# Optimization experiments

Measured on AMD Instinct MI355X. Metric: run time of the kernel, lower is better.

## Reference

```python
import jax, jax.numpy as jnp
import numpy as np

N = 500000      # total nodes
B = 10000       # number of graphs
D = 256         # node_size == global_size
SLOPE = 0.01    # LeakyReLU negative slope (torch default)

def leaky_relu(x):
    return jnp.where(x >= 0, x, SLOPE * x)

def setup_inputs() -> dict:
    key = jax.random.key(0)
    ks = jax.random.split(key, 10)
    xg_old = jax.random.normal(ks[0], (B, D), dtype=jnp.float32)
    x = jax.random.normal(ks[1], (N, D), dtype=jnp.float32)
    batch = jnp.sort(jax.random.randint(ks[2], (N,), 0, B)).astype(jnp.int64)
    s = 1.0 / np.sqrt(D)
    W_gate = jax.random.uniform(ks[3], (D, 1), minval=-s, maxval=s, dtype=jnp.float32)
    b_gate = jax.random.uniform(ks[4], (1,), minval=-s, maxval=s, dtype=jnp.float32)
    W_feat = jax.random.uniform(ks[5], (D, D), minval=-s, maxval=s, dtype=jnp.float32)
    b_feat = jax.random.uniform(ks[6], (D,), minval=-s, maxval=s, dtype=jnp.float32)
    s2 = 1.0 / np.sqrt(2 * D)
    W_t = jax.random.uniform(ks[7], (2 * D, D), minval=-s2, maxval=s2, dtype=jnp.float32)
    b_t = jax.random.uniform(ks[8], (D,), minval=-s2, maxval=s2, dtype=jnp.float32)
    return {"xg_old": xg_old, "x": x, "batch": batch,
            "W_gate": W_gate, "b_gate": b_gate,
            "W_feat": W_feat, "b_feat": b_feat,
            "W_t": W_t, "b_t": b_t}

def reference(xg_old, x, batch, W_gate, b_gate, W_feat, b_feat, W_t, b_t):
    batch = batch.astype(jnp.int32)
    # AttentionalAggregation: per-graph softmax over gate scores, weighted sum of feats
    gate = x @ W_gate + b_gate                               # [N, 1]
    feat = leaky_relu(x @ W_feat + b_feat)                   # [N, D]
    m = jax.ops.segment_max(gate, batch, num_segments=B)     # [B, 1]
    g = jnp.exp(gate - m[batch])                             # stable exp
    s = jax.ops.segment_sum(g, batch, num_segments=B)        # [B, 1]
    alpha = g / s[batch]                                     # [N, 1]
    xg = jax.ops.segment_sum(alpha * feat, batch, num_segments=B)  # [B, D]
    # concat with old global state, transform, residual
    cat = jnp.concatenate([xg, xg_old], axis=1)              # [B, 2D]
    out = leaky_relu(cat @ W_t + b_t) + xg_old               # [B, D]
    return out
```

## Files before the change

### kernel.cpp

```cpp
#include <hip/hip_runtime.h>
#include <hip/hip_bf16.h>
#include <math.h>

#define D 256
#define FT_STRIDE 72

typedef short v8s __attribute__((ext_vector_type(8)));
typedef float f32x4 __attribute__((ext_vector_type(4)));
typedef float f32x16 __attribute__((ext_vector_type(16)));

__device__ __forceinline__ unsigned short f2b(float f) {
    return __bfloat16_as_ushort(__float2bfloat16(f));
}
__device__ __forceinline__ float b2f(unsigned short u) {
    return __bfloat162float(__ushort_as_bfloat16(u));
}

__global__ void prep_kernel(const int* __restrict__ batch, int* __restrict__ seg_start,
                            const float* __restrict__ Wf, unsigned short* __restrict__ Wb32,
                            const float* __restrict__ Wt, unsigned short* __restrict__ Wtb,
                            float* __restrict__ xg, int N, int B) {
    const int blk = blockIdx.x, tid = threadIdx.x;
    if (blk < 40) {
        int b = blk * 256 + tid;
        if (b > B) return;
        int lo = 0, hi = N;
        while (lo < hi) {
            int mid = (lo + hi) >> 1;
            if (batch[mid] < b) lo = mid + 1; else hi = mid;
        }
        seg_start[b] = lo;
    } else if (blk < 296) {
        int idx = (blk - 40) * 256 + tid;
        int k = idx >> 8, n = idx & 255;
        int lane = ((k >> 3) & 1) * 32 + (n & 31);
        int j = k & 7, kst = k >> 4, ntile = n >> 5;
        Wb32[(((ntile * 16 + kst) * 64) + lane) * 8 + j] = f2b(Wf[k * 256 + n]);
    } else if (blk < 808) {
        int idx = (blk - 296) * 256 + tid;
        int k = idx >> 8, n = idx & 255;
        int ntile = n >> 4, kst = k >> 5;
        int lane = ((k >> 3) & 3) * 16 + (n & 15);
        int j = k & 7;
        Wtb[(((ntile * 16 + kst) * 64) + lane) * 8 + j] = f2b(Wt[k * 256 + n]);
    } else {
        int idx = (blk - 808) * 256 + tid;
        if (idx < 640000) ((float4*)xg)[idx] = make_float4(0.f, 0.f, 0.f, 0.f);
    }
}

template<bool CONV>
__global__ __launch_bounds__(256) void gate_conv_kernel(
    const float* __restrict__ x, const float* __restrict__ Wg,
    const float* __restrict__ bg, float* __restrict__ gate,
    unsigned short* __restrict__ xb16, int N) {
    const int lane = threadIdx.x & 63;
    const int wid = blockIdx.x * 4 + (threadIdx.x >> 6);
    const int nw = gridDim.x * 4;
    const float4 wv = *(const float4*)(Wg + lane * 4);
    const float bgv = bg[0];
    for (int n = wid * 2; n < N; n += nw * 2) {
        const float4 xv0 = *(const float4*)(x + (size_t)n * D + lane * 4);
        const float4 xv1 = *(const float4*)(x + (size_t)(n + 1) * D + lane * 4);
        if (CONV) {
            ushort4 h0 = { f2b(xv0.x), f2b(xv0.y), f2b(xv0.z), f2b(xv0.w) };
            ushort4 h1 = { f2b(xv1.x), f2b(xv1.y), f2b(xv1.z), f2b(xv1.w) };
            *(ushort4*)(xb16 + (size_t)n * D + lane * 4) = h0;
            *(ushort4*)(xb16 + (size_t)(n + 1) * D + lane * 4) = h1;
        }
        float d0 = xv0.x * wv.x + xv0.y * wv.y + xv0.z * wv.z + xv0.w * wv.w;
        float d1 = xv1.x * wv.x + xv1.y * wv.y + xv1.z * wv.z + xv1.w * wv.w;
        #pragma unroll
        for (int off = 32; off; off >>= 1) {
            d0 += __shfl_xor(d0, off, 64);
            d1 += __shfl_xor(d1, off, 64);
        }
        if (lane == 0) { gate[n] = d0 + bgv; gate[n + 1] = d1 + bgv; }
    }
}

__global__ __launch_bounds__(256) void stats_kernel(const float* __restrict__ gate,
                                                    const int* __restrict__ seg_start,
                                                    float* __restrict__ mvec,
                                                    float* __restrict__ invs, int B) {
    int wid = blockIdx.x * 4 + (threadIdx.x >> 6);
    int lane = threadIdx.x & 63;
    if (wid >= B) return;
    int s0 = seg_start[wid], s1 = seg_start[wid + 1];
    float m = -INFINITY;
    for (int i = s0 + lane; i < s1; i += 64) m = fmaxf(m, gate[i]);
    #pragma unroll
    for (int off = 32; off > 0; off >>= 1) m = fmaxf(m, __shfl_xor(m, off, 64));
    float s = 0.f;
    for (int i = s0 + lane; i < s1; i += 64) s += __expf(gate[i] - m);
    #pragma unroll
    for (int off = 32; off > 0; off >>= 1) s += __shfl_xor(s, off, 64);
    if (lane == 0) { mvec[wid] = m; invs[wid] = (s > 0.f) ? 1.f / s : 0.f; }
}

template<bool BF16IN>
__global__ __launch_bounds__(256, 4) void feat_attn_kernel(
    const float* __restrict__ x, const unsigned short* __restrict__ xb16,
    const unsigned short* __restrict__ Wb32,
    const float* __restrict__ bfeat, const float* __restrict__ gate,
    const int* __restrict__ batch, const float* __restrict__ mvec,
    const float* __restrict__ invs, float* __restrict__ xg, int N) {

    __shared__ unsigned short feat_s[256 * FT_STRIDE] __attribute__((aligned(16)));
    __shared__ float alpha_s[64];
    __shared__ int batch_s[64];

    const int tid = threadIdx.x;
    const int n0 = blockIdx.x * 64;

    if (tid < 64) {
        int n = n0 + tid;
        if (n < N) {
            int b = batch[n];
            batch_s[tid] = b;
            alpha_s[tid] = __expf(gate[n] - mvec[b]) * invs[b];
        } else {
            batch_s[tid] = batch[N - 1];
            alpha_s[tid] = 0.f;
        }
    }

    const int w = tid >> 6, lane = tid & 63;
    const int l31 = lane & 31, lh = lane >> 5;

    f32x16 acc[2][2];
    #pragma unroll
    for (int i = 0; i < 2; i++)
        #pragma unroll
        for (int j = 0; j < 2; j++)
            #pragma unroll
            for (int e = 0; e < 16; e++) acc[i][j][e] = 0.f;

    size_t abase[2];
    #pragma unroll
    for (int rt = 0; rt < 2; rt++) {
        int r = n0 + rt * 32 + l31;
        if (r > N - 1) r = N - 1;
        abase[rt] = (size_t)r * D + lh * 8;
    }

    v8s A[3][2], Bf[2][2];
    #pragma unroll
    for (int p = 0; p < 2; p++) {
        #pragma unroll
        for (int rt = 0; rt < 2; rt++) {
            if (BF16IN) A[p][rt] = *(const v8s*)(xb16 + abase[rt] + p * 16);
            else {
                const float* src = x + abase[rt] + p * 16;
                float4 f0 = *(const float4*)src, f1 = *(const float4*)(src + 4);
                v8s v; v[0]=(short)f2b(f0.x); v[1]=(short)f2b(f0.y);
                v[2]=(short)f2b(f0.z); v[3]=(short)f2b(f0.w);
                v[4]=(short)f2b(f1.x); v[5]=(short)f2b(f1.y);
                v[6]=(short)f2b(f1.z); v[7]=(short)f2b(f1.w);
                A[p][rt] = v;
            }
        }
        #pragma unroll
        for (int ct = 0; ct < 2; ct++)
            Bf[p][ct] = *(const v8s*)(Wb32 + (((size_t)(w * 2 + ct) * 16 + p) * 64 + lane) * 8);
    }

    #pragma unroll
    for (int ks = 0; ks < 16; ks++) {
        const int cs = ks % 3, bs = ks & 1;
        if (ks < 14) {
            const int ns = (ks + 2) % 3;
            #pragma unroll
            for (int rt = 0; rt < 2; rt++) {
                if (BF16IN) A[ns][rt] = *(const v8s*)(xb16 + abase[rt] + (ks + 2) * 16);
                else {
                    const float* src = x + abase[rt] + (ks + 2) * 16;
                    float4 f0 = *(const float4*)src, f1 = *(const float4*)(src + 4);
                    v8s v; v[0]=(short)f2b(f0.x); v[1]=(short)f2b(f0.y);
                    v[2]=(short)f2b(f0.z); v[3]=(short)f2b(f0.w);
                    v[4]=(short)f2b(f1.x); v[5]=(short)f2b(f1.y);
                    v[6]=(short)f2b(f1.z); v[7]=(short)f2b(f1.w);
                    A[ns][rt] = v;
                }
            }
        }
        if (ks < 15) {
            const int nb = (ks + 1) & 1;
            #pragma unroll
            for (int ct = 0; ct < 2; ct++)
                Bf[nb][ct] = *(const v8s*)(Wb32 + (((size_t)(w * 2 + ct) * 16 + ks + 1) * 64 + lane) * 8);
        }
        #pragma unroll
        for (int rt = 0; rt < 2; rt++)
            #pragma unroll
            for (int ct = 0; ct < 2; ct++)
                acc[rt][ct] = __builtin_amdgcn_mfma_f32_32x32x16_bf16(
                    A[cs][rt], Bf[bs][ct], acc[rt][ct], 0, 0, 0);
    }

    __syncthreads();

    #pragma unroll
    for (int ct = 0; ct < 2; ct++) {
        int col = w * 64 + ct * 32 + l31;
        float bias = bfeat[col];
        #pragma unroll
        for (int rt = 0; rt < 2; rt++) {
            #pragma unroll
            for (int g = 0; g < 4; g++) {
                int rbase = rt * 32 + g * 8 + 4 * lh;
                ushort4 h;
                #pragma unroll
                for (int rr = 0; rr < 4; rr++) {
                    float y = acc[rt][ct][g * 4 + rr] + bias;
                    y = (y >= 0.f) ? y : 0.01f * y;
                    y *= alpha_s[rbase + rr];
                    ((unsigned short*)&h)[rr] = f2b(y);
                }
                *(ushort4*)(&feat_s[col * FT_STRIDE + rbase]) = h;
            }
        }
    }
    __syncthreads();

    float sum = 0.f;
    int cur = batch_s[0];
    #pragma unroll
    for (int i0 = 0; i0 < 64; i0 += 8) {
        v8s f = *(const v8s*)(&feat_s[tid * FT_STRIDE + i0]);
        int b0 = batch_s[i0], b7 = batch_s[i0 + 7];
        if (b0 == b7) {
            if (b0 != cur) {
                atomicAdd(&xg[(size_t)cur * D + tid], sum);
                sum = 0.f; cur = b0;
            }
            float p0 = b2f((unsigned short)f[0]) + b2f((unsigned short)f[1]);
            float p1 = b2f((unsigned short)f[2]) + b2f((unsigned short)f[3]);
            float p2 = b2f((unsigned short)f[4]) + b2f((unsigned short)f[5]);
            float p3 = b2f((unsigned short)f[6]) + b2f((unsigned short)f[7]);
            sum += (p0 + p1) + (p2 + p3);
        } else {
            #pragma unroll
            for (int j = 0; j < 8; j++) {
                int b = batch_s[i0 + j];
                if (b != cur) {
                    atomicAdd(&xg[(size_t)cur * D + tid], sum);
                    sum = 0.f; cur = b;
                }
                sum += b2f((unsigned short)f[j]);
            }
        }
    }
    atomicAdd(&xg[(size_t)cur * D + tid], sum);
}

__global__ __launch_bounds__(256) void out_mfma_kernel(
    const float* __restrict__ xg, const float* __restrict__ xg_old,
    const unsigned short* __restrict__ Wtb, const float* __restrict__ bt,
    float* __restrict__ out, int B) {
    const int tid = threadIdx.x;
    const int w = tid >> 6, lane = tid & 63, mrow = lane & 15, q = lane >> 4;
    const int r0 = blockIdx.x * 64;

    f32x4 acc[4][4];
    #pragma unroll
    for (int i = 0; i < 4; i++)
        #pragma unroll
        for (int j = 0; j < 4; j++) acc[i][j] = (f32x4){0.f, 0.f, 0.f, 0.f};

    size_t rowbase[4];
    #pragma unroll
    for (int rb = 0; rb < 4; rb++) {
        int r = r0 + rb * 16 + mrow;
        if (r > B - 1) r = B - 1;
        rowbase[rb] = (size_t)r * D + q * 8;
    }

    #pragma unroll
    for (int ks = 0; ks < 16; ks++) {
        v8s a[4], bfr[4];
        #pragma unroll
        for (int rb = 0; rb < 4; rb++) {
            const float* src = (ks < 8) ? (xg + rowbase[rb] + ks * 32)
                                        : (xg_old + rowbase[rb] + (ks - 8) * 32);
            float4 f0 = *(const float4*)src;
            float4 f1 = *(const float4*)(src + 4);
            v8s v;
            v[0] = (short)f2b(f0.x); v[1] = (short)f2b(f0.y);
            v[2] = (short)f2b(f0.z); v[3] = (short)f2b(f0.w);
            v[4] = (short)f2b(f1.x); v[5] = (short)f2b(f1.y);
            v[6] = (short)f2b(f1.z); v[7] = (short)f2b(f1.w);
            a[rb] = v;
        }
        #pragma unroll
        for (int cb = 0; cb < 4; cb++)
            bfr[cb] = *(const v8s*)(Wtb + (((size_t)(w * 4 + cb) * 16 + ks) * 64 + lane) * 8);
        #pragma unroll
        for (int rb = 0; rb < 4; rb++)
            #pragma unroll
            for (int cb = 0; cb < 4; cb++)
                acc[rb][cb] = __builtin_amdgcn_mfma_f32_16x16x32_bf16(
                    a[rb], bfr[cb], acc[rb][cb], 0, 0, 0);
    }

    #pragma unroll
    for (int cb = 0; cb < 4; cb++) {
        int col = w * 64 + cb * 16 + mrow;
        float bias = bt[col];
        #pragma unroll
        for (int rb = 0; rb < 4; rb++) {
            #pragma unroll
            for (int reg = 0; reg < 4; reg++) {
                int row = r0 + rb * 16 + q * 4 + reg;
                if (row < B) {
                    float y = acc[rb][cb][reg] + bias;
                    y = (y >= 0.f) ? y : 0.01f * y;
                    out[(size_t)row * D + col] = y + xg_old[(size_t)row * D + col];
                }
            }
        }
    }
}

extern "C" void kernel_launch(void* const* d_in, const int* in_sizes, int n_in,
                              void* d_out, int out_size, void* d_ws, size_t ws_size,
                              hipStream_t stream) {
    const float* xg_old = (const float*)d_in[0];
    const float* x      = (const float*)d_in[1];
    const int*   batch  = (const int*)d_in[2];
    const float* W_gate = (const float*)d_in[3];
    const float* b_gate = (const float*)d_in[4];
    const float* W_feat = (const float*)d_in[5];
    const float* b_feat = (const float*)d_in[6];
    const float* W_t    = (const float*)d_in[7];
    const float* b_t    = (const float*)d_in[8];
    float* out = (float*)d_out;

    const int N = in_sizes[1] / D;
    const int B = in_sizes[0] / D;

    char* ws = (char*)d_ws;
    int*            seg_start = (int*)ws;
    float*          gate      = (float*)(ws + 0x10000);
    float*          mvec      = (float*)(ws + 0x220000);
    float*          invs      = (float*)(ws + 0x230000);
    unsigned short* Wb32      = (unsigned short*)(ws + 0x240000);
    unsigned short* Wtb       = (unsigned short*)(ws + 0x260000);
    float*          xg        = (float*)(ws + 0x2A0000);
    unsigned short* xb16      = (unsigned short*)(ws + 0xCA0000);

    const size_t need_full = 0xCA0000 + (size_t)N * D * 2;
    const bool full = ws_size >= need_full;

    prep_kernel<<<3308, 256, 0, stream>>>(batch, seg_start, W_feat, Wb32, W_t, Wtb, xg, N, B);
    if (full)
        gate_conv_kernel<true><<<2048, 256, 0, stream>>>(x, W_gate, b_gate, gate, xb16, N);
    else
        gate_conv_kernel<false><<<2048, 256, 0, stream>>>(x, W_gate, b_gate, gate, xb16, N);
    stats_kernel<<<(B + 3) / 4, 256, 0, stream>>>(gate, seg_start, mvec, invs, B);

    if (full)
        feat_attn_kernel<true><<<(N + 63) / 64, 256, 0, stream>>>(
            x, xb16, Wb32, b_feat, gate, batch, mvec, invs, xg, N);
    else
        feat_attn_kernel<false><<<(N + 63) / 64, 256, 0, stream>>>(
            x, xb16, Wb32, b_feat, gate, batch, mvec, invs, xg, N);

    out_mfma_kernel<<<(B + 63) / 64, 256, 0, stream>>>(xg, xg_old, Wtb, b_t, out, B);
}
```

Measured before the change: 955.0 us.

## Fuse gate and feature GEMM, stage bf16 features, then weighted-sum pass

Replaces the gate/bf16-conversion pass plus the combined feat+attention kernel with two kernels. The first reads x once, computing the gate dot product and the bf16 MFMA feature GEMM, and writes the activated features as bf16 tiles to a workspace buffer. After the stats kernel, a second kernel loads those tiles into LDS with global_load_lds and does the alpha-weighted segment sums with atomics. This drops the extra x read and the x bf16 copy, at the cost of writing and re-reading a roughly N*D*2-byte feature buffer.

New measurement: 1.214 ms. +27.2%, slower.

```diff
diff --git a/kernel.cpp b/kernel.cpp
--- a/kernel.cpp
+++ b/kernel.cpp
@@ -14,6 +14,12 @@
 }
 __device__ __forceinline__ float b2f(unsigned short u) {
     return __bfloat162float(__ushort_as_bfloat16(u));
+}
+
+__device__ __forceinline__ void gload16(const void* g, void* l) {
+    __builtin_amdgcn_global_load_lds(
+        (const __attribute__((address_space(1))) void*)g,
+        (__attribute__((address_space(3))) void*)l, 16, 0, 0);
 }
 
 __global__ void prep_kernel(const int* __restrict__ batch, int* __restrict__ seg_start,
@@ -98,6 +104,195 @@
     if (lane == 0) { mvec[wid] = m; invs[wid] = (s > 0.f) ? 1.f / s : 0.f; }
 }
 
+__global__ __launch_bounds__(256, 4) void featgate_kernel(
+    const float* __restrict__ x, const unsigned short* __restrict__ Wb32,
+    const float* __restrict__ Wg, const float* __restrict__ bg,
+    const float* __restrict__ bfeat, float* __restrict__ gate,
+    unsigned short* __restrict__ featbuf, int N) {
+
+    __shared__ unsigned short feat_s[256 * FT_STRIDE] __attribute__((aligned(16)));
+
+    const int tid = threadIdx.x;
+    const int n0 = blockIdx.x * 64;
+    const int w = tid >> 6, lane = tid & 63;
+    const int l31 = lane & 31, lh = lane >> 5;
+
+    f32x16 acc[2][2];
+    #pragma unroll
+    for (int i = 0; i < 2; i++)
+        #pragma unroll
+        for (int j = 0; j < 2; j++)
+            #pragma unroll
+            for (int e = 0; e < 16; e++) acc[i][j][e] = 0.f;
+
+    unsigned abase[2];
+    #pragma unroll
+    for (int rt = 0; rt < 2; rt++) {
+        int r = n0 + rt * 32 + l31;
+        if (r > N - 1) r = N - 1;
+        abase[rt] = (unsigned)r * D + lh * 8;
+    }
+
+    float gd0 = 0.f, gd1 = 0.f;
+    v8s A[3][2], Bf[2][2];
+
+    #define LOADA(s, k)                                                      \
+    {                                                                        \
+        _Pragma("unroll")                                                    \
+        for (int rt = 0; rt < 2; rt++) {                                     \
+            const float* src = x + abase[rt] + (k) * 16;                     \
+            float4 f0 = *(const float4*)src, f1 = *(const float4*)(src + 4); \
+            if (w == 0) {                                                    \
+                float4 g0 = *(const float4*)(Wg + lh * 8 + (k) * 16);        \
+                float4 g1 = *(const float4*)(Wg + lh * 8 + (k) * 16 + 4);    \
+                float t = f0.x * g0.x + f0.y * g0.y + f0.z * g0.z            \
+                        + f0.w * g0.w + f1.x * g1.x + f1.y * g1.y            \
+                        + f1.z * g1.z + f1.w * g1.w;                         \
+                if (rt == 0) gd0 += t; else gd1 += t;                        \
+            }                                                                \
+            v8s v;                                                           \
+            v[0] = (short)f2b(f0.x); v[1] = (short)f2b(f0.y);                \
+            v[2] = (short)f2b(f0.z); v[3] = (short)f2b(f0.w);                \
+            v[4] = (short)f2b(f1.x); v[5] = (short)f2b(f1.y);                \
+            v[6] = (short)f2b(f1.z); v[7] = (short)f2b(f1.w);                \
+            A[s][rt] = v;                                                    \
+        }                                                                    \
+    }
+
+    #pragma unroll
+    for (int p = 0; p < 2; p++) {
+        LOADA(p, p)
+        #pragma unroll
+        for (int ct = 0; ct < 2; ct++)
+            Bf[p][ct] = *(const v8s*)(Wb32 + (((size_t)(w * 2 + ct) * 16 + p) * 64 + lane) * 8);
+    }
+
+    #pragma unroll
+    for (int ks = 0; ks < 16; ks++) {
+        const int cs = ks % 3, bs = ks & 1;
+        if (ks < 14) LOADA((ks + 2) % 3, ks + 2)
+        if (ks < 15) {
+            const int nb = (ks + 1) & 1;
+            #pragma unroll
+            for (int ct = 0; ct < 2; ct++)
+                Bf[nb][ct] = *(const v8s*)(Wb32 + (((size_t)(w * 2 + ct) * 16 + ks + 1) * 64 + lane) * 8);
+        }
+        #pragma unroll
+        for (int rt = 0; rt < 2; rt++)
+            #pragma unroll
+            for (int ct = 0; ct < 2; ct++)
+                acc[rt][ct] = __builtin_amdgcn_mfma_f32_32x32x16_bf16(
+                    A[cs][rt], Bf[bs][ct], acc[rt][ct], 0, 0, 0);
+    }
+    #undef LOADA
+
+    if (w == 0) {
+        const float bgv = bg[0];
+        #pragma unroll
+        for (int rt = 0; rt < 2; rt++) {
+            float d = (rt == 0) ? gd0 : gd1;
+            d += __shfl_xor(d, 32, 64);
+            if (lh == 0) gate[abase[rt] >> 8] = d + bgv;
+        }
+    }
+
+    #pragma unroll
+    for (int ct = 0; ct < 2; ct++) {
+        int col = w * 64 + ct * 32 + l31;
+        float bias = bfeat[col];
+        #pragma unroll
+        for (int rt = 0; rt < 2; rt++) {
+            #pragma unroll
+            for (int g = 0; g < 4; g++) {
+                int rbase = rt * 32 + g * 8 + 4 * lh;
+                ushort4 h;
+                #pragma unroll
+                for (int rr = 0; rr < 4; rr++) {
+                    float y = acc[rt][ct][g * 4 + rr] + bias;
+                    y = (y >= 0.f) ? y : 0.01f * y;
+                    ((unsigned short*)&h)[rr] = f2b(y);
+                }
+                *(ushort4*)(&feat_s[col * FT_STRIDE + rbase]) = h;
+            }
+        }
+    }
+    __syncthreads();
+
+    unsigned short* dst = featbuf + (size_t)blockIdx.x * (256 * FT_STRIDE);
+    #pragma unroll
+    for (int it = 0; it < 9; it++) {
+        int off = it * 2048 + tid * 8;
+        *(v8s*)(dst + off) = *(const v8s*)(feat_s + off);
+    }
+}
+
+__global__ __launch_bounds__(256, 4) void wsum_kernel(
+    const unsigned short* __restrict__ featbuf, const float* __restrict__ gate,
+    const int* __restrict__ batch, const float* __restrict__ mvec,
+    const float* __restrict__ invs, float* __restrict__ xg, int N) {
+
+    __shared__ unsigned short feat_s[256 * FT_STRIDE] __attribute__((aligned(16)));
+    __shared__ float alpha_s[64];
+    __shared__ int batch_s[64];
+
+    const int tid = threadIdx.x;
+    const int n0 = blockIdx.x * 64;
+
+    const unsigned short* src = featbuf + (size_t)blockIdx.x * (256 * FT_STRIDE);
+    #pragma unroll
+    for (int it = 0; it < 9; it++) {
+        int off = it * 2048 + tid * 8;
+        gload16(src + off, feat_s + off);
+    }
+
+    if (tid < 64) {
+        int n = n0 + tid;
+        if (n < N) {
+            int b = batch[n];
+            batch_s[tid] = b;
+            alpha_s[tid] = __expf(gate[n] - mvec[b]) * invs[b];
+        } else {
+            batch_s[tid] = batch[N - 1];
+            alpha_s[tid] = 0.f;
+        }
+    }
+    __syncthreads();
+
+    float sum = 0.f;
+    int cur = batch_s[0];
+    #pragma unroll
+    for (int i0 = 0; i0 < 64; i0 += 8) {
+        v8s f = *(const v8s*)(&feat_s[tid * FT_STRIDE + i0]);
+        int b0 = batch_s[i0], b7 = batch_s[i0 + 7];
+        if (b0 == b7) {
+            if (b0 != cur) {
+                atomicAdd(&xg[(size_t)cur * D + tid], sum);
+                sum = 0.f; cur = b0;
+            }
+            float s0 = alpha_s[i0 + 0] * b2f((unsigned short)f[0])
+                     + alpha_s[i0 + 1] * b2f((unsigned short)f[1]);
+            float s1 = alpha_s[i0 + 2] * b2f((unsigned short)f[2])
+                     + alpha_s[i0 + 3] * b2f((unsigned short)f[3]);
+            float s2 = alpha_s[i0 + 4] * b2f((unsigned short)f[4])
+                     + alpha_s[i0 + 5] * b2f((unsigned short)f[5]);
+            float s3 = alpha_s[i0 + 6] * b2f((unsigned short)f[6])
+                     + alpha_s[i0 + 7] * b2f((unsigned short)f[7]);
+            sum += (s0 + s1) + (s2 + s3);
+        } else {
+            #pragma unroll
+            for (int j = 0; j < 8; j++) {
+                int b = batch_s[i0 + j];
+                if (b != cur) {
+                    atomicAdd(&xg[(size_t)cur * D + tid], sum);
+                    sum = 0.f; cur = b;
+                }
+                sum = fmaf(alpha_s[i0 + j], b2f((unsigned short)f[j]), sum);
+            }
+        }
+    }
+    atomicAdd(&xg[(size_t)cur * D + tid], sum);
+}
+
 template<bool BF16IN>
 __global__ __launch_bounds__(256, 4) void feat_attn_kernel(
     const float* __restrict__ x, const unsigned short* __restrict__ xb16,
@@ -338,6 +533,7 @@
 
     const int N = in_sizes[1] / D;
     const int B = in_sizes[0] / D;
+    const int nblk = (N + 63) / 64;
 
     char* ws = (char*)d_ws;
     int*            seg_start = (int*)ws;
@@ -347,24 +543,24 @@
     unsigned short* Wb32      = (unsigned short*)(ws + 0x240000);
     unsigned short* Wtb       = (unsigned short*)(ws + 0x260000);
     float*          xg        = (float*)(ws + 0x2A0000);
-    unsigned short* xb16      = (unsigned short*)(ws + 0xCA0000);
-
-    const size_t need_full = 0xCA0000 + (size_t)N * D * 2;
+    unsigned short* featbuf   = (unsigned short*)(ws + 0xCA0000);
+
+    const size_t need_full = 0xCA0000 + (size_t)nblk * (256 * FT_STRIDE * 2);
     const bool full = ws_size >= need_full;
 
     prep_kernel<<<3308, 256, 0, stream>>>(batch, seg_start, W_feat, Wb32, W_t, Wtb, xg, N, B);
-    if (full)
-        gate_conv_kernel<true><<<2048, 256, 0, stream>>>(x, W_gate, b_gate, gate, xb16, N);
-    else
-        gate_conv_kernel<false><<<2048, 256, 0, stream>>>(x, W_gate, b_gate, gate, xb16, N);
-    stats_kernel<<<(B + 3) / 4, 256, 0, stream>>>(gate, seg_start, mvec, invs, B);
-
-    if (full)
-        feat_attn_kernel<true><<<(N + 63) / 64, 256, 0, stream>>>(
-            x, xb16, Wb32, b_feat, gate, batch, mvec, invs, xg, N);
-    else
-        feat_attn_kernel<false><<<(N + 63) / 64, 256, 0, stream>>>(
-            x, xb16, Wb32, b_feat, gate, batch, mvec, invs, xg, N);
+
+    if (full) {
+        featgate_kernel<<<nblk, 256, 0, stream>>>(
+            x, Wb32, W_gate, b_gate, b_feat, gate, featbuf, N);
+        stats_kernel<<<(B + 3) / 4, 256, 0, stream>>>(gate, seg_start, mvec, invs, B);
+        wsum_kernel<<<nblk, 256, 0, stream>>>(featbuf, gate, batch, mvec, invs, xg, N);
+    } else {
+        gate_conv_kernel<false><<<2048, 256, 0, stream>>>(x, W_gate, b_gate, gate, nullptr, N);
+        stats_kernel<<<(B + 3) / 4, 256, 0, stream>>>(gate, seg_start, mvec, invs, B);
+        feat_attn_kernel<false><<<nblk, 256, 0, stream>>>(
+            x, nullptr, Wb32, b_feat, gate, batch, mvec, invs, xg, N);
+    }
 
     out_mfma_kernel<<<(B + 63) / 64, 256, 0, stream>>>(xg, xg_old, Wtb, b_t, out, B);
 }
```
